# Kernel tuning notes

Hardware: AMD Instinct MI355X
Metric: run time of the kernel (lower is better)

The kernel has to match this reference:

```python
import jax, jax.numpy as jnp
import numpy as np

K = 2  # number of propagation hops (init arg k)


def setup_inputs() -> dict:
    key = jax.random.key(0)
    k1, k2, k3 = jax.random.split(key, 3)
    N, E, D = 100000, 1200000, 64
    feat = jax.random.normal(k1, (N, D), dtype=jnp.float32)
    src = jax.random.randint(k2, (E,), 0, N, dtype=jnp.int32)
    dst = jax.random.randint(k3, (E,), 0, N, dtype=jnp.int32)
    return {"feat": feat, "src": src, "dst": dst, "n_nodes": N}


def reference(feat, src, dst, n_nodes):
    # in-degree normalization: norm = clamp(in_deg, 1)^-0.5, shape [N, 1]
    deg = jax.ops.segment_sum(
        jnp.ones(dst.shape, dtype=feat.dtype), dst, num_segments=n_nodes
    )
    norm = jnp.power(jnp.maximum(deg, 1.0), -0.5)[:, None]
    for _ in range(K):
        feat = feat * norm                      # pre-scale by D^-1/2
        msgs = feat[src]                        # copy_u: gather source features [E, D]
        feat = jax.ops.segment_sum(msgs, dst, num_segments=n_nodes)  # sum at dst
        feat = feat * norm                      # post-scale by D^-1/2
    return feat
```

## Files before the change

kernel.cpp:

```cpp
#include <hip/hip_runtime.h>
#include <hip/hip_fp16.h>

#define D 64
#define BSH2 8
#define NPB 256
#define NB2_MAX 512
#define PCHUNK 4096
#define CAPP 6144
#define CAP2 4096


__global__ void zero_f32(float* __restrict__ p, long n) {
    long i = (long)blockIdx.x * blockDim.x + threadIdx.x;
    long stride = (long)gridDim.x * blockDim.x;
    for (; i < n; i += stride) p[i] = 0.0f;
}

__global__ void init_cursors(int* __restrict__ gcur, int NB2) {
    int i = blockIdx.x * blockDim.x + threadIdx.x;
    if (i < NB2) gcur[i << 4] = i * CAPP;
}

__global__ __launch_bounds__(256) void feat_to_half_q(const float4* __restrict__ in,
                                                      const float* __restrict__ norm,
                                                      uint2* __restrict__ out, int N) {
    long i = (long)blockIdx.x * blockDim.x + threadIdx.x;
    long n4 = (long)N * 16;
    if (i < n4) {
        float4 v = in[i];
        int node = (int)(i >> 4);
        int t = (int)(i & 15);
        int q = t >> 2, j = t & 3;
        float r = norm[node];
        __half2 a = __floats2half2_rn(v.x * r, v.y * r);
        __half2 b = __floats2half2_rn(v.z * r, v.w * r);
        uint2 u;
        u.x = *(unsigned int*)&a;
        u.y = *(unsigned int*)&b;
        out[(long)q * N * 4 + node * 4 + j] = u;
    }
}

__global__ __launch_bounds__(1024) void partition_direct(const int* __restrict__ src,
                                                         const int* __restrict__ dst,
                                                         int* __restrict__ gcur,
                                                         int* __restrict__ packed,
                                                         int E, int NB2) {
    __shared__ int staged[PCHUNK];
    __shared__ int lhist[NB2_MAX];
    __shared__ int lbase[NB2_MAX];
    __shared__ int lcur[NB2_MAX];
    __shared__ int gbase[NB2_MAX];
    int tid = threadIdx.x;
    int c0 = blockIdx.x * PCHUNK;
    int c1 = c0 + PCHUNK; if (c1 > E) c1 = E;

    if (tid < NB2_MAX) lhist[tid] = 0;
    __syncthreads();

    for (int e = c0 + tid * 4; e + 4 <= c1; e += 4096) {
        int4 d4 = *(const int4*)(dst + e);
        atomicAdd(&lhist[d4.x >> BSH2], 1);
        atomicAdd(&lhist[d4.y >> BSH2], 1);
        atomicAdd(&lhist[d4.z >> BSH2], 1);
        atomicAdd(&lhist[d4.w >> BSH2], 1);
    }
    int tail = c0 + ((c1 - c0) & ~3);
    for (int e = tail + tid; e < c1; e += 1024)
        atomicAdd(&lhist[dst[e] >> BSH2], 1);
    __syncthreads();

    if (tid < 64) {
        const int CPL = NB2_MAX / 64;
        int tmp[CPL];
        int s = 0;
        int base = tid * CPL;
        #pragma unroll
        for (int j = 0; j < CPL; j++) { tmp[j] = s; s += lhist[base + j]; }
        int incl = s;
        #pragma unroll
        for (int o = 1; o < 64; o <<= 1) {
            int t = __shfl_up(incl, o, 64);
            if (tid >= o) incl += t;
        }
        int excl = incl - s;
        #pragma unroll
        for (int j = 0; j < CPL; j++) {
            lbase[base + j] = excl + tmp[j];
            lcur[base + j]  = excl + tmp[j];
        }
    }
    __syncthreads();

    for (int e = c0 + tid * 4; e + 4 <= c1; e += 4096) {
        int4 d4 = *(const int4*)(dst + e);
        int4 s4 = *(const int4*)(src + e);
        int k, pos;
        k = d4.x >> BSH2; pos = atomicAdd(&lcur[k], 1);
        staged[pos] = s4.x | ((d4.x & (NPB - 1)) << 20);
        k = d4.y >> BSH2; pos = atomicAdd(&lcur[k], 1);
        staged[pos] = s4.y | ((d4.y & (NPB - 1)) << 20);
        k = d4.z >> BSH2; pos = atomicAdd(&lcur[k], 1);
        staged[pos] = s4.z | ((d4.z & (NPB - 1)) << 20);
        k = d4.w >> BSH2; pos = atomicAdd(&lcur[k], 1);
        staged[pos] = s4.w | ((d4.w & (NPB - 1)) << 20);
    }
    for (int e = tail + tid; e < c1; e += 1024) {
        int d = dst[e];
        int k = d >> BSH2;
        int pos = atomicAdd(&lcur[k], 1);
        staged[pos] = src[e] | ((d & (NPB - 1)) << 20);
    }
    __syncthreads();

    if (tid < NB2_MAX && tid < NB2) {
        int c = lhist[tid];
        gbase[tid] = c ? atomicAdd(&gcur[tid << 4], (c + 15) & ~15) : 0;
    }
    __syncthreads();

    int grp = tid >> 4, sub = tid & 15;
    for (int k = grp; k < NB2; k += 64) {
        int c = lhist[k];
        if (!c) continue;
        int c16 = (c + 15) & ~15;
        int g = gbase[k], base = lbase[k];
        for (int i = sub; i < c16; i += 16)
            packed[g + i] = (i < c) ? staged[base + i] : -1;
    }
}

__global__ __launch_bounds__(1024) void bucket_csr(const int* __restrict__ packed,
                                                   const int* __restrict__ gcur,
                                                   int2* __restrict__ rbc,
                                                   float* __restrict__ norm,
                                                   float* __restrict__ norm2,
                                                   int* __restrict__ csr,
                                                   int N, int NB2) {
    __shared__ int cnt[NPB];
    __shared__ int loc[NPB];
    int b = blockIdx.x;
    int tid = threadIdx.x;
    if (tid < NPB) cnt[tid] = 0;
    __syncthreads();

    int rbeg = b * CAPP;
    int rend = gcur[b << 4];
    for (int e = rbeg + tid * 4; e + 4 <= rend; e += 4096) {
        int4 p4 = *(const int4*)(packed + e);
        if (p4.x != -1) atomicAdd(&cnt[(p4.x >> 20) & (NPB - 1)], 1);
        if (p4.y != -1) atomicAdd(&cnt[(p4.y >> 20) & (NPB - 1)], 1);
        if (p4.z != -1) atomicAdd(&cnt[(p4.z >> 20) & (NPB - 1)], 1);
        if (p4.w != -1) atomicAdd(&cnt[(p4.w >> 20) & (NPB - 1)], 1);
    }
    __syncthreads();
    if (tid < 64) {
        int tmp[4];
        int s = 0;
        int base = tid * 4;
        #pragma unroll
        for (int j = 0; j < 4; j++) { tmp[j] = s; s += cnt[base + j]; }
        int incl = s;
        #pragma unroll
        for (int o = 1; o < 64; o <<= 1) {
            int t = __shfl_up(incl, o, 64);
            if (tid >= o) incl += t;
        }
        int excl = incl - s;
        #pragma unroll
        for (int j = 0; j < 4; j++) loc[base + j] = excl + tmp[j];
    }
    __syncthreads();

    int cbase = b * CAP2;
    if (tid < NPB) {
        int node = (b << BSH2) + tid;
        if (node < N) {
            int v = cnt[tid];
            int ep = loc[tid];
            rbc[node] = make_int2(cbase + ep, v);
            float df = (float)v; df = df < 1.0f ? 1.0f : df;
            float r = rsqrtf(df);
            norm[node] = r;
            norm2[node] = r * r;
        }
    }
    __syncthreads();
    for (int e = rbeg + tid * 4; e + 4 <= rend; e += 4096) {
        int4 p4 = *(const int4*)(packed + e);
        int l, pos;
        if (p4.x != -1) { l = (p4.x >> 20) & (NPB - 1); pos = atomicAdd(&loc[l], 1); csr[cbase + pos] = p4.x & 0xFFFFF; }
        if (p4.y != -1) { l = (p4.y >> 20) & (NPB - 1); pos = atomicAdd(&loc[l], 1); csr[cbase + pos] = p4.y & 0xFFFFF; }
        if (p4.z != -1) { l = (p4.z >> 20) & (NPB - 1); pos = atomicAdd(&loc[l], 1); csr[cbase + pos] = p4.z & 0xFFFFF; }
        if (p4.w != -1) { l = (p4.w >> 20) & (NPB - 1); pos = atomicAdd(&loc[l], 1); csr[cbase + pos] = p4.w & 0xFFFFF; }
    }
}

template <bool OUTHALF>
__global__ __launch_bounds__(256) void gather_pull(const __half* __restrict__ xq,
                                                   const int2* __restrict__ rbc,
                                                   const int* __restrict__ csr,
                                                   const float* __restrict__ post,
                                                   void* __restrict__ outv,
                                                   int N, int nbq) {
    int q = blockIdx.x / nbq;
    int b = blockIdx.x - q * nbq;
    int grp = threadIdx.x >> 1;
    int sub = threadIdx.x & 1;
    int w = b * 128 + grp;
    if (w >= N) return;
    int2 bc = rbc[w];
    int beg = bc.x, end = bc.x + bc.y;
    const uint4* x16 = ((const uint4*)xq) + (long)q * N * 2;

    float a0 = 0.f, a1 = 0.f, a2 = 0.f, a3 = 0.f;
    float a4 = 0.f, a5 = 0.f, a6 = 0.f, a7 = 0.f;

    for (int e = beg; e < end; e += 4) {
        int e1 = e + 1, e2 = e + 2, e3 = e + 3;
        float m1 = (e1 < end) ? 1.f : 0.f; if (e1 >= end) e1 = end - 1;
        float m2 = (e2 < end) ? 1.f : 0.f; if (e2 >= end) e2 = end - 1;
        float m3 = (e3 < end) ? 1.f : 0.f; if (e3 >= end) e3 = end - 1;
        int s0 = csr[e];
        int s1 = csr[e1];
        int s2 = csr[e2];
        int s3 = csr[e3];
        uint4 u0 = x16[s0 * 2 + sub];
        uint4 u1 = x16[s1 * 2 + sub];
        uint4 u2 = x16[s2 * 2 + sub];
        uint4 u3 = x16[s3 * 2 + sub];
        float2 f;
        f = __half22float2(*(const __half2*)&u0.x); a0 += f.x; a1 += f.y;
        f = __half22float2(*(const __half2*)&u0.y); a2 += f.x; a3 += f.y;
        f = __half22float2(*(const __half2*)&u0.z); a4 += f.x; a5 += f.y;
        f = __half22float2(*(const __half2*)&u0.w); a6 += f.x; a7 += f.y;
        f = __half22float2(*(const __half2*)&u1.x); a0 += f.x * m1; a1 += f.y * m1;
        f = __half22float2(*(const __half2*)&u1.y); a2 += f.x * m1; a3 += f.y * m1;
        f = __half22float2(*(const __half2*)&u1.z); a4 += f.x * m1; a5 += f.y * m1;
        f = __half22float2(*(const __half2*)&u1.w); a6 += f.x * m1; a7 += f.y * m1;
        f = __half22float2(*(const __half2*)&u2.x); a0 += f.x * m2; a1 += f.y * m2;
        f = __half22float2(*(const __half2*)&u2.y); a2 += f.x * m2; a3 += f.y * m2;
        f = __half22float2(*(const __half2*)&u2.z); a4 += f.x * m2; a5 += f.y * m2;
        f = __half22float2(*(const __half2*)&u2.w); a6 += f.x * m2; a7 += f.y * m2;
        f = __half22float2(*(const __half2*)&u3.x); a0 += f.x * m3; a1 += f.y * m3;
        f = __half22float2(*(const __half2*)&u3.y); a2 += f.x * m3; a3 += f.y * m3;
        f = __half22float2(*(const __half2*)&u3.z); a4 += f.x * m3; a5 += f.y * m3;
        f = __half22float2(*(const __half2*)&u3.w); a6 += f.x * m3; a7 += f.y * m3;
    }

    float pn = post[w];
    a0 *= pn; a1 *= pn; a2 *= pn; a3 *= pn;
    a4 *= pn; a5 *= pn; a6 *= pn; a7 *= pn;
    if (OUTHALF) {
        __half2 h0 = __floats2half2_rn(a0, a1);
        __half2 h1 = __floats2half2_rn(a2, a3);
        __half2 h2 = __floats2half2_rn(a4, a5);
        __half2 h3 = __floats2half2_rn(a6, a7);
        uint4 u;
        u.x = *(unsigned int*)&h0;
        u.y = *(unsigned int*)&h1;
        u.z = *(unsigned int*)&h2;
        u.w = *(unsigned int*)&h3;
        ((uint4*)outv)[(long)q * N * 2 + (long)w * 2 + sub] = u;
    } else {
        float4 r0; r0.x = a0; r0.y = a1; r0.z = a2; r0.w = a3;
        float4 r1; r1.x = a4; r1.y = a5; r1.z = a6; r1.w = a7;
        ((float4*)outv)[(long)w * 16 + q * 4 + sub * 2]     = r0;
        ((float4*)outv)[(long)w * 16 + q * 4 + sub * 2 + 1] = r1;
    }
}


__global__ void deg_kernel_f(const int* __restrict__ dst, float* __restrict__ deg, int E) {
    int e = blockIdx.x * blockDim.x + threadIdx.x;
    if (e < E) unsafeAtomicAdd(&deg[dst[e]], 1.0f);
}

__global__ void norm_kernel_f(float* __restrict__ deg_norm, float* __restrict__ norm2, int N) {
    int i = blockIdx.x * blockDim.x + threadIdx.x;
    if (i < N) {
        float d = deg_norm[i];
        d = d < 1.0f ? 1.0f : d;
        float r = rsqrtf(d);
        deg_norm[i] = r;
        norm2[i] = r * r;
    }
}

__global__ void scatter_kernel(const float* __restrict__ x,
                               const float* __restrict__ scale,
                               const int* __restrict__ src,
                               const int* __restrict__ dst,
                               float* __restrict__ out, int E) {
    long idx = (long)blockIdx.x * blockDim.x + threadIdx.x;
    int e = (int)(idx >> 6);
    int lane = (int)(idx & 63);
    if (e < E) {
        int s = src[e];
        int d0 = dst[e];
        float v = x[(long)s * D + lane] * scale[s];
        unsafeAtomicAdd(&out[(long)d0 * D + lane], v);
    }
}

__global__ void scale_kernel(float* __restrict__ out, const float* __restrict__ norm, long n) {
    long i = (long)blockIdx.x * blockDim.x + threadIdx.x;
    if (i < n) out[i] *= norm[i >> 6];
}


extern "C" void kernel_launch(void* const* d_in, const int* in_sizes, int n_in,
                              void* d_out, int out_size, void* d_ws, size_t ws_size,
                              hipStream_t stream) {
    const float* feat = (const float*)d_in[0];
    const int*   src  = (const int*)d_in[1];
    const int*   dst  = (const int*)d_in[2];
    float* out = (float*)d_out;

    const int N = in_sizes[0] / D;
    const int E = in_sizes[1];
    const long ND = (long)N * D;
    const int NB2 = (N + NPB - 1) >> BSH2;

    long o_gcur = 0;
    long o_rbc  = o_gcur + NB2_MAX * 16;
    long o_norm = o_rbc + 2L * N;
    long o_norm2 = o_norm + N;
    long o_csr  = (o_norm2 + N + 3) & ~3L;
    long o_f16  = (o_csr + (long)NB2 * CAP2 + 3) & ~3L;
    long o_buf1 = (o_f16 + ND / 2 + 3) & ~3L;
    long pk_len = (long)NB2 * CAPP;
    long buf1_len = (ND / 2 > pk_len) ? ND / 2 : pk_len;
    size_t need = (size_t)(o_buf1 + buf1_len) * 4;

    if (ws_size >= need && N <= (1 << 20) && NB2 <= NB2_MAX) {
        int*   bi = (int*)d_ws;
        float* bf = (float*)d_ws;
        int* gcur    = bi + o_gcur;
        int2* rbc    = (int2*)(bi + o_rbc);
        float* norm  = bf + o_norm;
        float* norm2 = bf + o_norm2;
        int* csr     = bi + o_csr;
        __half* feat16 = (__half*)(bi + o_f16);
        __half* buf1h  = (__half*)(bi + o_buf1);
        int* packed  = bi + o_buf1;

        int pblocks = (E + PCHUNK - 1) / PCHUNK;

        init_cursors<<<(NB2 + 255) / 256, 256, 0, stream>>>(gcur, NB2);
        partition_direct<<<pblocks, 1024, 0, stream>>>(src, dst, gcur, packed, E, NB2);
        bucket_csr<<<NB2, 1024, 0, stream>>>(packed, gcur, rbc, norm, norm2, csr, N, NB2);
        long n4 = ND / 4;
        feat_to_half_q<<<(int)((n4 + 255) / 256), 256, 0, stream>>>(
            (const float4*)feat, norm, (uint2*)feat16, N);

        int nbq = (N + 127) / 128;
        gather_pull<true><<<nbq * 4, 256, 0, stream>>>(feat16, rbc, csr, norm2, buf1h, N, nbq);
        gather_pull<false><<<nbq * 4, 256, 0, stream>>>(buf1h, rbc, csr, norm, out, N, nbq);
    } else {
        float* norm  = (float*)d_ws;
        float* norm2 = norm + N;
        float* buf1  = norm2 + N;

        long nz = 2L * N + ND;
        zero_f32<<<(int)((nz + 255) / 256), 256, 0, stream>>>((float*)d_ws, nz);
        zero_f32<<<(int)((ND + 255) / 256), 256, 0, stream>>>(out, ND);
        deg_kernel_f<<<(E + 255) / 256, 256, 0, stream>>>(dst, norm, E);
        norm_kernel_f<<<(N + 255) / 256, 256, 0, stream>>>(norm, norm2, N);
        long work = (long)E * D;
        int blocks = (int)((work + 255) / 256);
        scatter_kernel<<<blocks, 256, 0, stream>>>(feat, norm, src, dst, buf1, E);
        scatter_kernel<<<blocks, 256, 0, stream>>>(buf1, norm2, src, dst, out, E);
        scale_kernel<<<(int)((ND + 255) / 256), 256, 0, stream>>>(out, norm, ND);
    }
}
```

Baseline: 198.0 us.

## Fuse half conversion into CSR build, XCD-aware block mapping, unroll gather by eight

After: 207.7 us. 4.9% more time.

```diff
diff --git a/kernel.cpp b/kernel.cpp
--- a/kernel.cpp
+++ b/kernel.cpp
@@ -9,6 +9,9 @@
 #define CAPP 6144
 #define CAP2 4096
 
+typedef unsigned int uint32x4 __attribute__((ext_vector_type(4)));
+typedef float f32x4 __attribute__((ext_vector_type(4)));
+
 
 __global__ void zero_f32(float* __restrict__ p, long n) {
     long i = (long)blockIdx.x * blockDim.x + threadIdx.x;
@@ -19,26 +22,6 @@
 __global__ void init_cursors(int* __restrict__ gcur, int NB2) {
     int i = blockIdx.x * blockDim.x + threadIdx.x;
     if (i < NB2) gcur[i << 4] = i * CAPP;
-}
-
-__global__ __launch_bounds__(256) void feat_to_half_q(const float4* __restrict__ in,
-                                                      const float* __restrict__ norm,
-                                                      uint2* __restrict__ out, int N) {
-    long i = (long)blockIdx.x * blockDim.x + threadIdx.x;
-    long n4 = (long)N * 16;
-    if (i < n4) {
-        float4 v = in[i];
-        int node = (int)(i >> 4);
-        int t = (int)(i & 15);
-        int q = t >> 2, j = t & 3;
-        float r = norm[node];
-        __half2 a = __floats2half2_rn(v.x * r, v.y * r);
-        __half2 b = __floats2half2_rn(v.z * r, v.w * r);
-        uint2 u;
-        u.x = *(unsigned int*)&a;
-        u.y = *(unsigned int*)&b;
-        out[(long)q * N * 4 + node * 4 + j] = u;
-    }
 }
 
 __global__ __launch_bounds__(1024) void partition_direct(const int* __restrict__ src,
@@ -136,6 +119,8 @@
                                                    float* __restrict__ norm,
                                                    float* __restrict__ norm2,
                                                    int* __restrict__ csr,
+                                                   const float4* __restrict__ feat,
+                                                   uint2* __restrict__ fq,
                                                    int N, int NB2) {
     __shared__ int cnt[NPB];
     __shared__ int loc[NPB];
@@ -194,6 +179,26 @@
         if (p4.z != -1) { l = (p4.z >> 20) & (NPB - 1); pos = atomicAdd(&loc[l], 1); csr[cbase + pos] = p4.z & 0xFFFFF; }
         if (p4.w != -1) { l = (p4.w >> 20) & (NPB - 1); pos = atomicAdd(&loc[l], 1); csr[cbase + pos] = p4.w & 0xFFFFF; }
     }
+
+    #pragma unroll
+    for (int it = 0; it < 4; it++) {
+        int item = tid + it * 1024;
+        int l = item >> 4;
+        int node = (b << BSH2) + l;
+        if (node < N) {
+            int t = item & 15;
+            int q = t >> 2, j = t & 3;
+            float4 v = feat[(long)node * 16 + t];
+            float df = (float)cnt[l]; df = df < 1.0f ? 1.0f : df;
+            float r = rsqrtf(df);
+            __half2 a = __floats2half2_rn(v.x * r, v.y * r);
+            __half2 bb = __floats2half2_rn(v.z * r, v.w * r);
+            uint2 u;
+            u.x = *(unsigned int*)&a;
+            u.y = *(unsigned int*)&bb;
+            fq[(long)q * N * 4 + (long)node * 4 + j] = u;
+        }
+    }
 }
 
 template <bool OUTHALF>
@@ -202,12 +207,14 @@
                                                    const int* __restrict__ csr,
                                                    const float* __restrict__ post,
                                                    void* __restrict__ outv,
-                                                   int N, int nbq) {
-    int q = blockIdx.x / nbq;
-    int b = blockIdx.x - q * nbq;
+                                                   int N) {
+    int bid = blockIdx.x;
+    int xcd = bid & 7;
+    int q = xcd & 3;
+    int chunk = ((bid >> 3) << 1) + (xcd >> 2);
     int grp = threadIdx.x >> 1;
     int sub = threadIdx.x & 1;
-    int w = b * 128 + grp;
+    int w = chunk * 128 + grp;
     if (w >= N) return;
     int2 bc = rbc[w];
     int beg = bc.x, end = bc.x + bc.y;
@@ -216,37 +223,62 @@
     float a0 = 0.f, a1 = 0.f, a2 = 0.f, a3 = 0.f;
     float a4 = 0.f, a5 = 0.f, a6 = 0.f, a7 = 0.f;
 
-    for (int e = beg; e < end; e += 4) {
-        int e1 = e + 1, e2 = e + 2, e3 = e + 3;
-        float m1 = (e1 < end) ? 1.f : 0.f; if (e1 >= end) e1 = end - 1;
-        float m2 = (e2 < end) ? 1.f : 0.f; if (e2 >= end) e2 = end - 1;
-        float m3 = (e3 < end) ? 1.f : 0.f; if (e3 >= end) e3 = end - 1;
-        int s0 = csr[e];
-        int s1 = csr[e1];
-        int s2 = csr[e2];
-        int s3 = csr[e3];
+#define ACC8(u, m) { float2 f_; \
+    f_ = __half22float2(*(const __half2*)&(u).x); a0 += f_.x * (m); a1 += f_.y * (m); \
+    f_ = __half22float2(*(const __half2*)&(u).y); a2 += f_.x * (m); a3 += f_.y * (m); \
+    f_ = __half22float2(*(const __half2*)&(u).z); a4 += f_.x * (m); a5 += f_.y * (m); \
+    f_ = __half22float2(*(const __half2*)&(u).w); a6 += f_.x * (m); a7 += f_.y * (m); }
+
+    int e = beg;
+    for (; e + 8 <= end; e += 8) {
+        int s0 = __builtin_nontemporal_load(csr + e + 0);
+        int s1 = __builtin_nontemporal_load(csr + e + 1);
+        int s2 = __builtin_nontemporal_load(csr + e + 2);
+        int s3 = __builtin_nontemporal_load(csr + e + 3);
+        int s4 = __builtin_nontemporal_load(csr + e + 4);
+        int s5 = __builtin_nontemporal_load(csr + e + 5);
+        int s6 = __builtin_nontemporal_load(csr + e + 6);
+        int s7 = __builtin_nontemporal_load(csr + e + 7);
         uint4 u0 = x16[s0 * 2 + sub];
         uint4 u1 = x16[s1 * 2 + sub];
         uint4 u2 = x16[s2 * 2 + sub];
         uint4 u3 = x16[s3 * 2 + sub];
-        float2 f;
-        f = __half22float2(*(const __half2*)&u0.x); a0 += f.x; a1 += f.y;
-        f = __half22float2(*(const __half2*)&u0.y); a2 += f.x; a3 += f.y;
-        f = __half22float2(*(const __half2*)&u0.z); a4 += f.x; a5 += f.y;
-        f = __half22float2(*(const __half2*)&u0.w); a6 += f.x; a7 += f.y;
-        f = __half22float2(*(const __half2*)&u1.x); a0 += f.x * m1; a1 += f.y * m1;
-        f = __half22float2(*(const __half2*)&u1.y); a2 += f.x * m1; a3 += f.y * m1;
-        f = __half22float2(*(const __half2*)&u1.z); a4 += f.x * m1; a5 += f.y * m1;
-        f = __half22float2(*(const __half2*)&u1.w); a6 += f.x * m1; a7 += f.y * m1;
-        f = __half22float2(*(const __half2*)&u2.x); a0 += f.x * m2; a1 += f.y * m2;
-        f = __half22float2(*(const __half2*)&u2.y); a2 += f.x * m2; a3 += f.y * m2;
-        f = __half22float2(*(const __half2*)&u2.z); a4 += f.x * m2; a5 += f.y * m2;
-        f = __half22float2(*(const __half2*)&u2.w); a6 += f.x * m2; a7 += f.y * m2;
-        f = __half22float2(*(const __half2*)&u3.x); a0 += f.x * m3; a1 += f.y * m3;
-        f = __half22float2(*(const __half2*)&u3.y); a2 += f.x * m3; a3 += f.y * m3;
-        f = __half22float2(*(const __half2*)&u3.z); a4 += f.x * m3; a5 += f.y * m3;
-        f = __half22float2(*(const __half2*)&u3.w); a6 += f.x * m3; a7 += f.y * m3;
-    }
+        uint4 u4 = x16[s4 * 2 + sub];
+        uint4 u5 = x16[s5 * 2 + sub];
+        uint4 u6 = x16[s6 * 2 + sub];
+        uint4 u7 = x16[s7 * 2 + sub];
+        ACC8(u0, 1.f) ACC8(u1, 1.f) ACC8(u2, 1.f) ACC8(u3, 1.f)
+        ACC8(u4, 1.f) ACC8(u5, 1.f) ACC8(u6, 1.f) ACC8(u7, 1.f)
+    }
+    if (e < end) {
+        int i1 = e + 1, i2 = e + 2, i3 = e + 3, i4 = e + 4, i5 = e + 5, i6 = e + 6, i7 = e + 7;
+        float m1 = (i1 < end) ? 1.f : 0.f; if (i1 >= end) i1 = end - 1;
+        float m2 = (i2 < end) ? 1.f : 0.f; if (i2 >= end) i2 = end - 1;
+        float m3 = (i3 < end) ? 1.f : 0.f; if (i3 >= end) i3 = end - 1;
+        float m4 = (i4 < end) ? 1.f : 0.f; if (i4 >= end) i4 = end - 1;
+        float m5 = (i5 < end) ? 1.f : 0.f; if (i5 >= end) i5 = end - 1;
+        float m6 = (i6 < end) ? 1.f : 0.f; if (i6 >= end) i6 = end - 1;
+        float m7 = (i7 < end) ? 1.f : 0.f; if (i7 >= end) i7 = end - 1;
+        int s0 = __builtin_nontemporal_load(csr + e);
+        int s1 = __builtin_nontemporal_load(csr + i1);
+        int s2 = __builtin_nontemporal_load(csr + i2);
+        int s3 = __builtin_nontemporal_load(csr + i3);
+        int s4 = __builtin_nontemporal_load(csr + i4);
+        int s5 = __builtin_nontemporal_load(csr + i5);
+        int s6 = __builtin_nontemporal_load(csr + i6);
+        int s7 = __builtin_nontemporal_load(csr + i7);
+        uint4 u0 = x16[s0 * 2 + sub];
+        uint4 u1 = x16[s1 * 2 + sub];
+        uint4 u2 = x16[s2 * 2 + sub];
+        uint4 u3 = x16[s3 * 2 + sub];
+        uint4 u4 = x16[s4 * 2 + sub];
+        uint4 u5 = x16[s5 * 2 + sub];
+        uint4 u6 = x16[s6 * 2 + sub];
+        uint4 u7 = x16[s7 * 2 + sub];
+        ACC8(u0, 1.f) ACC8(u1, m1) ACC8(u2, m2) ACC8(u3, m3)
+        ACC8(u4, m4)  ACC8(u5, m5) ACC8(u6, m6) ACC8(u7, m7)
+    }
+#undef ACC8
 
     float pn = post[w];
     a0 *= pn; a1 *= pn; a2 *= pn; a3 *= pn;
@@ -256,17 +288,17 @@
         __half2 h1 = __floats2half2_rn(a2, a3);
         __half2 h2 = __floats2half2_rn(a4, a5);
         __half2 h3 = __floats2half2_rn(a6, a7);
-        uint4 u;
+        uint32x4 u;
         u.x = *(unsigned int*)&h0;
         u.y = *(unsigned int*)&h1;
         u.z = *(unsigned int*)&h2;
         u.w = *(unsigned int*)&h3;
-        ((uint4*)outv)[(long)q * N * 2 + (long)w * 2 + sub] = u;
+        __builtin_nontemporal_store(u, ((uint32x4*)outv) + (long)q * N * 2 + (long)w * 2 + sub);
     } else {
-        float4 r0; r0.x = a0; r0.y = a1; r0.z = a2; r0.w = a3;
-        float4 r1; r1.x = a4; r1.y = a5; r1.z = a6; r1.w = a7;
-        ((float4*)outv)[(long)w * 16 + q * 4 + sub * 2]     = r0;
-        ((float4*)outv)[(long)w * 16 + q * 4 + sub * 2 + 1] = r1;
+        f32x4 r0; r0.x = a0; r0.y = a1; r0.z = a2; r0.w = a3;
+        f32x4 r1; r1.x = a4; r1.y = a5; r1.z = a6; r1.w = a7;
+        __builtin_nontemporal_store(r0, ((f32x4*)outv) + (long)w * 16 + q * 4 + sub * 2);
+        __builtin_nontemporal_store(r1, ((f32x4*)outv) + (long)w * 16 + q * 4 + sub * 2 + 1);
     }
 }
 
@@ -349,14 +381,14 @@
 
         init_cursors<<<(NB2 + 255) / 256, 256, 0, stream>>>(gcur, NB2);
         partition_direct<<<pblocks, 1024, 0, stream>>>(src, dst, gcur, packed, E, NB2);
-        bucket_csr<<<NB2, 1024, 0, stream>>>(packed, gcur, rbc, norm, norm2, csr, N, NB2);
-        long n4 = ND / 4;
-        feat_to_half_q<<<(int)((n4 + 255) / 256), 256, 0, stream>>>(
-            (const float4*)feat, norm, (uint2*)feat16, N);
-
-        int nbq = (N + 127) / 128;
-        gather_pull<true><<<nbq * 4, 256, 0, stream>>>(feat16, rbc, csr, norm2, buf1h, N, nbq);
-        gather_pull<false><<<nbq * 4, 256, 0, stream>>>(buf1h, rbc, csr, norm, out, N, nbq);
+        bucket_csr<<<NB2, 1024, 0, stream>>>(packed, gcur, rbc, norm, norm2, csr,
+                                             (const float4*)feat, (uint2*)feat16, N, NB2);
+
+        int NC = (N + 127) / 128;
+        int B8 = (NC + 1) / 2;
+        int grid = B8 * 8;
+        gather_pull<true><<<grid, 256, 0, stream>>>(feat16, rbc, csr, norm2, buf1h, N);
+        gather_pull<false><<<grid, 256, 0, stream>>>(buf1h, rbc, csr, norm, out, N);
     } else {
         float* norm  = (float*)d_ws;
         float* norm2 = norm + N;
```
